# Performance work log

Hardware: AMD Instinct MI355X
Metric: run time of the kernel (lower is better)

## Reference

```python
import jax, jax.numpy as jnp
import numpy as np

N, D, C = 8192, 512, 1000


def setup_inputs() -> dict:
    key = jax.random.key(0)
    k1, k2, k3 = jax.random.split(key, 3)
    features = jax.random.normal(k1, (N, D), dtype=jnp.float32)
    centers = jax.random.normal(k2, (C, D), dtype=jnp.float32)
    labels = jax.random.randint(k3, (N,), 0, C, dtype=jnp.int64)
    return {"features": features, "centers": centers, "labels": labels}


def _l2_normalize(x, axis=1, eps=1e-12):
    # matches torch F.normalize(p=2): x / max(||x||, eps)
    norm = jnp.sqrt(jnp.sum(x * x, axis=axis, keepdims=True))
    return x / jnp.maximum(norm, eps)


def reference(features, centers, labels):
    f = _l2_normalize(features, axis=1)          # [N, D]
    c = _l2_normalize(centers, axis=1)           # [C, D]
    centers_batch = c[labels]                    # [N, D]
    pos_distances = 1.0 - jnp.sum(f * centers_batch, axis=1)      # [N]
    neg_distances = 1.0 - jnp.matmul(f, f.T)                       # [N, N]
    losses = pos_distances[:, None] - neg_distances                # [N, N]
    diff_class = labels[:, None] != labels[None, :]                # [N, N]
    valid = diff_class & (losses > 0.0)                            # [N, N]
    losses = jnp.where(valid, losses, 0.0)
    num_valid_pairs = jnp.sum(valid, axis=1)                       # [N]
    num_valid_pairs = jnp.where(num_valid_pairs > 0, num_valid_pairs, 1)
    sample_losses = jnp.sum(losses, axis=1) / num_valid_pairs.astype(losses.dtype)
    num_valid_samples = jnp.sum(sample_losses > 0.0)
    loss = jnp.sum(sample_losses)
    loss = jnp.where(num_valid_samples > 0,
                     loss / num_valid_samples.astype(loss.dtype), loss)
    return loss
```

## Files before the change

### kernel.cpp

```cpp
#include <hip/hip_runtime.h>
#include <hip/hip_bf16.h>
#include <hip/hip_fp8.h>
#include <stdint.h>
#include <math.h>

#define N_ROWS 8192
#define DIM    512
#define BM     256
#define BK     64
#define NB     (N_ROWS / BM)
#define NTRI   (NB * (NB + 1) / 2)
#define NKT    (DIM / BK)

typedef float f32x4 __attribute__((ext_vector_type(4)));
typedef long  lng2  __attribute__((ext_vector_type(2)));


__global__ __launch_bounds__(256) void k_prep(const float* __restrict__ feats,
                                              const float* __restrict__ centers,
                                              const int* __restrict__ labels,
                                              unsigned char* __restrict__ f_q,
                                              float* __restrict__ posdot,
                                              float* __restrict__ Ssum,
                                              int* __restrict__ Kcnt) {
    const int row = blockIdx.x;
    const int t = threadIdx.x;
    const float* src = feats + (size_t)row * DIM;
    float v0 = src[t], v1 = src[t + 256];
    float ss = v0 * v0 + v1 * v1;
#pragma unroll
    for (int m = 1; m < 64; m <<= 1) ss += __shfl_xor(ss, m, 64);
    __shared__ float red[12];
    const int lane = t & 63, wid = t >> 6;
    if (lane == 0) red[wid] = ss;
    __syncthreads();
    const float tot = red[0] + red[1] + red[2] + red[3];
    const float scale = 1.0f / fmaxf(sqrtf(tot), 1e-12f);
    const float n0 = v0 * scale, n1 = v1 * scale;
    {
        __hip_fp8_e4m3 q0(n0), q1(n1);
#pragma unroll
        for (int j = 0; j < 2; ++j) {
            const int k  = t + j * 256;
            const int kt = k >> 6, k6 = k & 63;
            const int h  = (k6 >> 5) & 1;
            const int u  = (k6 >> 3) & 3;
            const int pos = kt * 64 + u * 16 + h * 8 + (k6 & 7);
            const unsigned char qb = (j == 0) ? *reinterpret_cast<const unsigned char*>(&q0)
                                              : *reinterpret_cast<const unsigned char*>(&q1);
            f_q[(size_t)row * DIM + pos] = qb;
        }
    }

    const int lab = labels[row];
    const float* c = centers + (size_t)lab * DIM;
    const float c0 = c[t], c1 = c[t + 256];
    float cc = c0 * c0 + c1 * c1;
    float d  = n0 * c0 + n1 * c1;
#pragma unroll
    for (int m = 1; m < 64; m <<= 1) {
        cc += __shfl_xor(cc, m, 64);
        d  += __shfl_xor(d, m, 64);
    }
    if (lane == 0) { red[4 + wid] = cc; red[8 + wid] = d; }
    __syncthreads();
    if (t == 0) {
        const float ctot = red[4] + red[5] + red[6] + red[7];
        const float dtot = red[8] + red[9] + red[10] + red[11];
        posdot[row] = dtot / fmaxf(sqrtf(ctot), 1e-12f);
        Ssum[row] = 0.0f;
        Kcnt[row] = 0;
    }
}

__global__ __launch_bounds__(512) void k_pair(const unsigned char* __restrict__ f_q,
                                              const int* __restrict__ labels,
                                              const float* __restrict__ pd,
                                              float* __restrict__ Ssum,
                                              int* __restrict__ Kcnt) {
    __shared__ __align__(16) unsigned char sA[4][BM * BK];
    __shared__ __align__(16) unsigned char sB[4][BM * BK];
    __shared__ int   s_lr[BM];
    __shared__ int   s_lc[BM];
    __shared__ float s_pd[BM];
    __shared__ float s_pc[BM];

    const int tid  = threadIdx.x;
    const int lane = tid & 63;
    const int wid  = tid >> 6;
    const int wr   = wid >> 2;
    const int wc   = wid & 3;

    const int t = blockIdx.x;
    int bi = (int)floor((2.0 * NB + 1.0 - sqrt((2.0 * NB + 1.0) * (2.0 * NB + 1.0) - 8.0 * (double)t)) * 0.5);
    while (bi * NB - bi * (bi - 1) / 2 > t) --bi;
    while ((bi + 1) * NB - (bi + 1) * bi / 2 <= t) ++bi;
    const int bj = bi + (t - (bi * NB - bi * (bi - 1) / 2));
    const int rowBase = bi * BM;
    const int colBase = bj * BM;
    const bool offdiag = (bi != bj);

    if (tid < BM) {
        s_lr[tid] = labels[rowBase + tid];
        s_pd[tid] = pd[rowBase + tid];
    } else {
        s_lc[tid - BM] = labels[colBase + tid - BM];
        s_pc[tid - BM] = pd[colBase + tid - BM];
    }

    f32x4 acc[8][4] = {};

    const int srow = lane >> 2;
    const int slu  = (lane & 3) ^ ((lane >> 3) & 3);

#define STAGE(KT, P)                                                                       \
    do {                                                                                   \
        const int k0_ = (KT) * BK;                                                         \
        _Pragma("unroll")                                                                  \
        for (int i_ = 0; i_ < 2; ++i_) {                                                   \
            const int ch_ = wid * 2 + i_;                                                  \
            const int r_  = ch_ * 16 + srow;                                               \
            const unsigned char* gA_ = f_q + ((size_t)(rowBase + r_) * DIM + k0_ + slu * 16); \
            const unsigned char* gB_ = f_q + ((size_t)(colBase + r_) * DIM + k0_ + slu * 16); \
            __builtin_amdgcn_global_load_lds(                                              \
                (const __attribute__((address_space(1))) void*)gA_,                        \
                (__attribute__((address_space(3))) void*)(&sA[P][ch_ * 1024]), 16, 0, 0);  \
            __builtin_amdgcn_global_load_lds(                                              \
                (const __attribute__((address_space(1))) void*)gB_,                        \
                (__attribute__((address_space(3))) void*)(&sB[P][ch_ * 1024]), 16, 0, 0);  \
        }                                                                                  \
    } while (0)

    const int pu = (lane >> 4) ^ ((lane >> 1) & 3);

    STAGE(0, 0);
    STAGE(1, 1);
    STAGE(2, 2);
    asm volatile("s_waitcnt vmcnt(8)" ::: "memory");
    __builtin_amdgcn_s_barrier();
    __builtin_amdgcn_sched_barrier(0);

#pragma unroll
    for (int kt = 0; kt < NKT; ++kt) {
        const int P = kt & 3;
        if (kt <= 4) STAGE(kt + 3, (kt + 3) & 3);

        lng2 aF[8], bF[4];
#pragma unroll
        for (int m = 0; m < 8; ++m) {
            const int r = wr * 128 + m * 16 + (lane & 15);
            aF[m] = *(const lng2*)(&sA[P][r * 64 + pu * 16]);
        }
#pragma unroll
        for (int n = 0; n < 4; ++n) {
            const int r = wc * 64 + n * 16 + (lane & 15);
            bF[n] = *(const lng2*)(&sB[P][r * 64 + pu * 16]);
        }

        __builtin_amdgcn_s_setprio(1);
#pragma unroll
        for (int m = 0; m < 8; ++m)
#pragma unroll
            for (int n = 0; n < 4; ++n) {
                acc[m][n] = __builtin_amdgcn_mfma_f32_16x16x32_fp8_fp8(aF[m].x, bF[n].x, acc[m][n], 0, 0, 0);
                acc[m][n] = __builtin_amdgcn_mfma_f32_16x16x32_fp8_fp8(aF[m].y, bF[n].y, acc[m][n], 0, 0, 0);
            }
        __builtin_amdgcn_s_setprio(0);

        if (kt < 5) {
            asm volatile("s_waitcnt vmcnt(8)" ::: "memory");
            __builtin_amdgcn_s_barrier();
            __builtin_amdgcn_sched_barrier(0);
        } else if (kt == 5) {
            asm volatile("s_waitcnt vmcnt(4)" ::: "memory");
            __builtin_amdgcn_s_barrier();
            __builtin_amdgcn_sched_barrier(0);
        } else if (kt == 6) {
            asm volatile("s_waitcnt vmcnt(0)" ::: "memory");
            __builtin_amdgcn_s_barrier();
            __builtin_amdgcn_sched_barrier(0);
        }
    }

#undef STAGE

    float colS[4] = {0.f, 0.f, 0.f, 0.f};
    int   colK[4] = {0, 0, 0, 0};
    int   lcv[4]; float pcv[4];
#pragma unroll
    for (int n = 0; n < 4; ++n) {
        const int jl = wc * 64 + n * 16 + (lane & 15);
        lcv[n] = s_lc[jl];
        pcv[n] = s_pc[jl];
    }

#pragma unroll
    for (int m = 0; m < 8; ++m) {
        float rowS[4] = {0.f, 0.f, 0.f, 0.f};
        int   rowK[4] = {0, 0, 0, 0};
        const int rloc = wr * 128 + m * 16 + ((lane >> 4) << 2);
        int myLr[4]; float myPd[4];
#pragma unroll
        for (int g = 0; g < 4; ++g) { myLr[g] = s_lr[rloc + g]; myPd[g] = s_pd[rloc + g]; }
#pragma unroll
        for (int n = 0; n < 4; ++n) {
#pragma unroll
            for (int g = 0; g < 4; ++g) {
                const float s = acc[m][n][g];
                const bool diff = (myLr[g] != lcv[n]);
                if (diff && s > myPd[g]) { rowS[g] += (s - myPd[g]); rowK[g] += 1; }
                if (offdiag && diff && s > pcv[n]) { colS[n] += (s - pcv[n]); colK[n] += 1; }
            }
        }
#pragma unroll
        for (int g = 0; g < 4; ++g) {
#pragma unroll
            for (int d = 1; d < 16; d <<= 1) {
                rowS[g] += __shfl_xor(rowS[g], d, 64);
                rowK[g] += __shfl_xor(rowK[g], d, 64);
            }
        }
        if ((lane & 15) == 0) {
#pragma unroll
            for (int g = 0; g < 4; ++g) {
                const int r = rowBase + rloc + g;
                atomicAdd(&Ssum[r], rowS[g]);
                atomicAdd(&Kcnt[r], rowK[g]);
            }
        }
    }

    if (offdiag) {
#pragma unroll
        for (int n = 0; n < 4; ++n) {
#pragma unroll
            for (int d = 16; d < 64; d <<= 1) {
                colS[n] += __shfl_xor(colS[n], d, 64);
                colK[n] += __shfl_xor(colK[n], d, 64);
            }
        }
        if (lane < 16) {
#pragma unroll
            for (int n = 0; n < 4; ++n) {
                const int c = colBase + wc * 64 + n * 16 + lane;
                atomicAdd(&Ssum[c], colS[n]);
                atomicAdd(&Kcnt[c], colK[n]);
            }
        }
    }
}

__global__ __launch_bounds__(1024) void k_final(const float* __restrict__ Ssum,
                                                const int* __restrict__ Kcnt,
                                                float* __restrict__ out) {
    const int t = threadIdx.x;
    double sum = 0.0; int cnt = 0;
    for (int i = t; i < N_ROWS; i += 1024) {
        const int k = Kcnt[i];
        if (k > 0) { sum += (double)Ssum[i] / (double)k; cnt += 1; }
    }
#pragma unroll
    for (int d = 1; d < 64; d <<= 1) {
        sum += __shfl_xor(sum, d, 64);
        cnt += __shfl_xor(cnt, d, 64);
    }
    __shared__ double s_sum[16];
    __shared__ int    s_cnt[16];
    const int lane = t & 63, wid = t >> 6;
    if (lane == 0) { s_sum[wid] = sum; s_cnt[wid] = cnt; }
    __syncthreads();
    if (t == 0) {
        double ts = 0.0; int tc = 0;
#pragma unroll
        for (int w = 0; w < 16; ++w) { ts += s_sum[w]; tc += s_cnt[w]; }
        out[0] = (float)(tc > 0 ? ts / (double)tc : ts);
    }
}

extern "C" void kernel_launch(void* const* d_in, const int* in_sizes, int n_in,
                              void* d_out, int out_size, void* d_ws, size_t ws_size,
                              hipStream_t stream) {
    const float* features = (const float*)d_in[0];
    const float* centers  = (const float*)d_in[1];
    const int*   labels   = (const int*)d_in[2];
    float* out = (float*)d_out;

    char* ws = (char*)d_ws;
    unsigned char* f_q    = (unsigned char*)(ws);
    float*         posdot = (float*)(ws + 0x400000);
    float*         Ssum   = (float*)(ws + 0x400000 + 0x8000);
    int*           Kcnt   = (int*)  (ws + 0x400000 + 0x10000);

    k_prep<<<N_ROWS, 256, 0, stream>>>(features, centers, labels, f_q, posdot, Ssum, Kcnt);
    k_pair<<<NTRI, 512, 0, stream>>>(f_q, labels, posdot, Ssum, Kcnt);
    k_final<<<1, 1024, 0, stream>>>(Ssum, Kcnt, out);
}
```

Measured before the change: 103.0 us.

## Split each K-step into four phases interleaving LDS reads, prefetch and MFMA

Each K tile's compute is split into four sub-phases, each covering a quarter of the 8x4 accumulator grid. Every phase loads only its A/B fragments from LDS and, in the first two phases, issues one half of the next stage's global-to-LDS prefetch. Barriers now sit between phases in a ping-pong style schedule so LDS reads, global loads and MFMA bursts from different waves overlap. The cost is many more barriers per K step (about four instead of one) and some repeated fragment loads.

```diff
diff --git a/kernel.cpp b/kernel.cpp
--- a/kernel.cpp
+++ b/kernel.cpp
@@ -113,76 +113,73 @@
     const int srow = lane >> 2;
     const int slu  = (lane & 3) ^ ((lane >> 3) & 3);
 
-#define STAGE(KT, P)                                                                       \
+#define STAGE1(KT, P, I)                                                                   \
     do {                                                                                   \
         const int k0_ = (KT) * BK;                                                         \
-        _Pragma("unroll")                                                                  \
-        for (int i_ = 0; i_ < 2; ++i_) {                                                   \
-            const int ch_ = wid * 2 + i_;                                                  \
-            const int r_  = ch_ * 16 + srow;                                               \
-            const unsigned char* gA_ = f_q + ((size_t)(rowBase + r_) * DIM + k0_ + slu * 16); \
-            const unsigned char* gB_ = f_q + ((size_t)(colBase + r_) * DIM + k0_ + slu * 16); \
-            __builtin_amdgcn_global_load_lds(                                              \
-                (const __attribute__((address_space(1))) void*)gA_,                        \
-                (__attribute__((address_space(3))) void*)(&sA[P][ch_ * 1024]), 16, 0, 0);  \
-            __builtin_amdgcn_global_load_lds(                                              \
-                (const __attribute__((address_space(1))) void*)gB_,                        \
-                (__attribute__((address_space(3))) void*)(&sB[P][ch_ * 1024]), 16, 0, 0);  \
-        }                                                                                  \
+        const int ch_ = wid * 2 + (I);                                                     \
+        const int r_  = ch_ * 16 + srow;                                                   \
+        const unsigned char* gA_ = f_q + ((size_t)(rowBase + r_) * DIM + k0_ + slu * 16);  \
+        const unsigned char* gB_ = f_q + ((size_t)(colBase + r_) * DIM + k0_ + slu * 16);  \
+        __builtin_amdgcn_global_load_lds(                                                  \
+            (const __attribute__((address_space(1))) void*)gA_,                            \
+            (__attribute__((address_space(3))) void*)(&sA[P][ch_ * 1024]), 16, 0, 0);      \
+        __builtin_amdgcn_global_load_lds(                                                  \
+            (const __attribute__((address_space(1))) void*)gB_,                            \
+            (__attribute__((address_space(3))) void*)(&sB[P][ch_ * 1024]), 16, 0, 0);      \
     } while (0)
 
     const int pu = (lane >> 4) ^ ((lane >> 1) & 3);
 
-    STAGE(0, 0);
-    STAGE(1, 1);
-    STAGE(2, 2);
-    asm volatile("s_waitcnt vmcnt(8)" ::: "memory");
+    STAGE1(0, 0, 0); STAGE1(0, 0, 1);
+    STAGE1(1, 1, 0); STAGE1(1, 1, 1);
+    STAGE1(2, 2, 0); STAGE1(2, 2, 1);
+    asm volatile("s_waitcnt vmcnt(8) lgkmcnt(0)" ::: "memory");
     __builtin_amdgcn_s_barrier();
     __builtin_amdgcn_sched_barrier(0);
 
 #pragma unroll
     for (int kt = 0; kt < NKT; ++kt) {
         const int P = kt & 3;
-        if (kt <= 4) STAGE(kt + 3, (kt + 3) & 3);
-
-        lng2 aF[8], bF[4];
-#pragma unroll
-        for (int m = 0; m < 8; ++m) {
-            const int r = wr * 128 + m * 16 + (lane & 15);
-            aF[m] = *(const lng2*)(&sA[P][r * 64 + pu * 16]);
-        }
-#pragma unroll
-        for (int n = 0; n < 4; ++n) {
-            const int r = wc * 64 + n * 16 + (lane & 15);
-            bF[n] = *(const lng2*)(&sB[P][r * 64 + pu * 16]);
-        }
-
-        __builtin_amdgcn_s_setprio(1);
-#pragma unroll
-        for (int m = 0; m < 8; ++m)
-#pragma unroll
-            for (int n = 0; n < 4; ++n) {
-                acc[m][n] = __builtin_amdgcn_mfma_f32_16x16x32_fp8_fp8(aF[m].x, bF[n].x, acc[m][n], 0, 0, 0);
-                acc[m][n] = __builtin_amdgcn_mfma_f32_16x16x32_fp8_fp8(aF[m].y, bF[n].y, acc[m][n], 0, 0, 0);
-            }
-        __builtin_amdgcn_s_setprio(0);
-
-        if (kt < 5) {
-            asm volatile("s_waitcnt vmcnt(8)" ::: "memory");
+#pragma unroll
+        for (int ph = 0; ph < 4; ++ph) {
+            const int mh = ph >> 1, nh = ph & 1;
+            lng2 aF[4], bF[2];
+#pragma unroll
+            for (int mi = 0; mi < 4; ++mi) {
+                const int r = wr * 128 + (mh * 4 + mi) * 16 + (lane & 15);
+                aF[mi] = *(const lng2*)(&sA[P][r * 64 + pu * 16]);
+            }
+#pragma unroll
+            for (int ni = 0; ni < 2; ++ni) {
+                const int r = wc * 64 + (nh * 2 + ni) * 16 + (lane & 15);
+                bF[ni] = *(const lng2*)(&sB[P][r * 64 + pu * 16]);
+            }
+            if (kt <= 4 && ph < 2) STAGE1(kt + 3, (kt + 3) & 3, ph);
+
             __builtin_amdgcn_s_barrier();
+            asm volatile("s_waitcnt lgkmcnt(0)" ::: "memory");
             __builtin_amdgcn_sched_barrier(0);
-        } else if (kt == 5) {
-            asm volatile("s_waitcnt vmcnt(4)" ::: "memory");
-            __builtin_amdgcn_s_barrier();
-            __builtin_amdgcn_sched_barrier(0);
-        } else if (kt == 6) {
-            asm volatile("s_waitcnt vmcnt(0)" ::: "memory");
-            __builtin_amdgcn_s_barrier();
-            __builtin_amdgcn_sched_barrier(0);
-        }
-    }
-
-#undef STAGE
+            __builtin_amdgcn_s_setprio(1);
+#pragma unroll
+            for (int mi = 0; mi < 4; ++mi)
+#pragma unroll
+                for (int ni = 0; ni < 2; ++ni) {
+                    f32x4& a = acc[mh * 4 + mi][nh * 2 + ni];
+                    a = __builtin_amdgcn_mfma_f32_16x16x32_fp8_fp8(aF[mi].x, bF[ni].x, a, 0, 0, 0);
+                    a = __builtin_amdgcn_mfma_f32_16x16x32_fp8_fp8(aF[mi].y, bF[ni].y, a, 0, 0, 0);
+                }
+            __builtin_amdgcn_s_setprio(0);
+
+            if (ph == 3) {
+                if (kt < 5)       asm volatile("s_waitcnt vmcnt(8)" ::: "memory");
+                else if (kt == 5) asm volatile("s_waitcnt vmcnt(4)" ::: "memory");
+                else if (kt == 6) asm volatile("s_waitcnt vmcnt(0)" ::: "memory");
+            }
+            if (!(kt == NKT - 1 && ph == 3)) __builtin_amdgcn_s_barrier();
+        }
+    }
+
+#undef STAGE1
 
     float colS[4] = {0.f, 0.f, 0.f, 0.f};
     int   colK[4] = {0, 0, 0, 0};
```

New measurement: 110.3 us. 1.07x slower.
